# Performance work log

Measured on AMD Instinct MI355X. Metric: run time of the kernel, lower is better.

## Reference

```python
import jax, jax.numpy as jnp
import numpy as np
import math

D = 2048
NH = 16
DH = D // NH
LAT = D // 4
B, S = 2, 2048
EPS = 1e-5


def _ln(x, g, b):
    m = jnp.mean(x, axis=-1, keepdims=True)
    v = jnp.mean((x - m) ** 2, axis=-1, keepdims=True)
    return (x - m) * jax.lax.rsqrt(v + EPS) * g + b


def setup_inputs() -> dict:
    key = jax.random.key(0)
    ks = jax.random.split(key, 12)
    p = lambda k, shape: 0.01 * jax.random.normal(k, shape, dtype=jnp.float32)
    return {
        "x": jax.random.normal(ks[0], (B, S, D), dtype=jnp.float32),
        "W_dq": p(ks[1], (D, LAT)),
        "W_uq": p(ks[2], (LAT, D)),
        "q_ln_g": jnp.ones((LAT,), jnp.float32),
        "q_ln_b": jnp.zeros((LAT,), jnp.float32),
        "W_dkv": p(ks[3], (D, LAT)),
        "W_ukv": p(ks[4], (LAT, 2 * D)),
        "kv_ln_g": jnp.ones((LAT,), jnp.float32),
        "kv_ln_b": jnp.zeros((LAT,), jnp.float32),
        "W_o": p(ks[5], (D, D)),
        "norm1_g": jnp.ones((D,), jnp.float32),
        "norm1_b": jnp.zeros((D,), jnp.float32),
        "norm2_g": jnp.ones((D,), jnp.float32),
        "norm2_b": jnp.zeros((D,), jnp.float32),
        "fc1_w": p(ks[6], (4 * D, D)),
        "fc1_b": jnp.zeros((4 * D,), jnp.float32),
        "fc2_w": p(ks[7], (D, 4 * D)),
        "fc2_b": jnp.zeros((D,), jnp.float32),
    }


def reference(x, W_dq, W_uq, q_ln_g, q_ln_b, W_dkv, W_ukv, kv_ln_g, kv_ln_b,
              W_o, norm1_g, norm1_b, norm2_g, norm2_b, fc1_w, fc1_b, fc2_w, fc2_b):
    normed = _ln(x, norm1_g, norm1_b)

    # --- RopelessMLA attention ---
    cq = _ln(normed @ W_dq, q_ln_g, q_ln_b)          # [B,S,LAT]
    Q = cq @ W_uq                                     # [B,S,D]
    ckv = _ln(normed @ W_dkv, kv_ln_g, kv_ln_b)       # [B,S,LAT]
    KV = ckv @ W_ukv                                  # [B,S,2D]
    K, V = KV[..., :D], KV[..., D:]

    q = Q.reshape(B, S, NH, DH)
    k = K.reshape(B, S, NH, DH)
    v = V.reshape(B, S, NH, DH)

    qkt = jnp.einsum("bqhd,bkhd->bhqk", q, k) / math.sqrt(float(DH))
    mask = jnp.tril(jnp.ones((S, S), dtype=qkt.dtype))  # causal, past_length=0
    qkt = qkt * mask
    qkt = jnp.where(qkt == 0.0, -jnp.inf, qkt)  # faithful to original zero->-inf trick
    attn = jax.nn.softmax(qkt, axis=-1)
    o = jnp.einsum("bhqk,bkhd->bqhd", attn, v).reshape(B, S, D)
    mh_x = o @ W_o.T

    x = x + mh_x
    h = _ln(x, norm2_g, norm2_b)
    h = jax.nn.relu(h @ fc1_w.T + fc1_b)
    h = h @ fc2_w.T + fc2_b  # dropout is identity in eval mode
    return x + h
```

## Files before the change

### kernel.cpp

```cpp
#include <hip/hip_runtime.h>
#include <hip/hip_bf16.h>


#define DEVI __device__ __forceinline__

typedef __attribute__((ext_vector_type(8))) short bf16x8;
typedef __attribute__((ext_vector_type(4))) float f32x4;

DEVI unsigned short f2bf(float f) {
  union { float f; unsigned u; } v; v.f = f;
  unsigned r = v.u + 0x7fffu + ((v.u >> 16) & 1u);
  return (unsigned short)(r >> 16);
}

DEVI float bf2f(unsigned short u) {
  union { unsigned u; float f; } v; v.u = ((unsigned)u) << 16;
  return v.f;
}

#define GLDS16(gp, lp)                                              \
  __builtin_amdgcn_global_load_lds(                                 \
      (__attribute__((address_space(1))) void*)(gp),                \
      (__attribute__((address_space(3))) void*)(lp), 16, 0, 0)

#define NEG_INF (-__builtin_inff())

__global__ __launch_bounds__(256) void cast_f32_bf16(
    const float* __restrict__ in, unsigned short* __restrict__ out, long n) {
  long i = ((long)blockIdx.x * 256 + threadIdx.x) * 4;
  if (i >= n) return;
  const float4 v = *reinterpret_cast<const float4*>(in + i);
  ushort4 o;
  o.x = f2bf(v.x); o.y = f2bf(v.y); o.z = f2bf(v.z); o.w = f2bf(v.w);
  *reinterpret_cast<ushort4*>(out + i) = o;
}

__global__ __launch_bounds__(256) void transpose_cast(
    const float* __restrict__ in, unsigned short* __restrict__ out, int R, int C) {
  __shared__ float tile[32][33];
  const int c0 = blockIdx.x * 32, r0 = blockIdx.y * 32;
  const int tx = threadIdx.x & 31, ty = threadIdx.x >> 5;
#pragma unroll
  for (int i = 0; i < 32; i += 8)
    tile[ty + i][tx] = in[(long)(r0 + ty + i) * C + c0 + tx];
  __syncthreads();
#pragma unroll
  for (int i = 0; i < 32; i += 8)
    out[(long)(c0 + ty + i) * R + r0 + tx] = f2bf(tile[tx][ty + i]);
}

__global__ __launch_bounds__(256) void v_transpose(
    const unsigned short* __restrict__ KV, unsigned short* __restrict__ Vt) {
  __shared__ unsigned short sh[32][33];
  const int s0 = blockIdx.x * 32, d0 = blockIdx.y * 32, bh = blockIdx.z;
  const int b = bh >> 4, h = bh & 15;
  const int tx = threadIdx.x & 31, ty = threadIdx.x >> 5;
#pragma unroll
  for (int i = 0; i < 32; i += 8)
    sh[ty + i][tx] = KV[((long)(b * 2048 + s0 + ty + i)) * 4096 + 2048 + h * 128 + d0 + tx];
  __syncthreads();
#pragma unroll
  for (int i = 0; i < 32; i += 8)
    Vt[((long)(bh * 128 + d0 + ty + i)) * 2048 + s0 + tx] = sh[tx][ty + i];
}

DEVI float blockReduceSum(float v) {
  v += __shfl_xor(v, 1);  v += __shfl_xor(v, 2);  v += __shfl_xor(v, 4);
  v += __shfl_xor(v, 8);  v += __shfl_xor(v, 16); v += __shfl_xor(v, 32);
  __shared__ float red[4];
  if ((threadIdx.x & 63) == 0) red[threadIdx.x >> 6] = v;
  __syncthreads();
  v = red[0] + red[1] + red[2] + red[3];
  __syncthreads();
  return v;
}

template <int W>
__global__ __launch_bounds__(256) void layernorm_bf16(
    const float* __restrict__ in, const float* __restrict__ g,
    const float* __restrict__ b, unsigned short* __restrict__ out, int ldin) {
  constexpr int VPT = W / 256;
  const long row = blockIdx.x;
  const float* x = in + row * ldin;
  float v[VPT];
  float s = 0.f;
#pragma unroll
  for (int i = 0; i < VPT; i++) { v[i] = x[threadIdx.x + i * 256]; s += v[i]; }
  s = blockReduceSum(s);
  const float mean = s * (1.0f / W);
  float s2 = 0.f;
#pragma unroll
  for (int i = 0; i < VPT; i++) { float d = v[i] - mean; s2 += d * d; }
  s2 = blockReduceSum(s2);
  const float rstd = rsqrtf(s2 * (1.0f / W) + 1e-5f);
#pragma unroll
  for (int i = 0; i < VPT; i++) {
    const int c = threadIdx.x + i * 256;
    out[row * W + c] = f2bf((v[i] - mean) * rstd * g[c] + b[c]);
  }
}

template <bool BIAS, bool RELU, bool RES, bool OBF16>
__global__ __launch_bounds__(256) void gemm_bt(
    const unsigned short* __restrict__ A, const unsigned short* __restrict__ Bt,
    const float* __restrict__ bias, const float* __restrict__ res,
    void* __restrict__ Cout, int M, int N, int K) {
  __shared__ __align__(16) unsigned short As[2][128 * 32];
  __shared__ __align__(16) unsigned short Bs[2][128 * 32];

  const int m0 = blockIdx.x * 128;
  const int n0 = blockIdx.y * 128;
  const int tid = threadIdx.x;
  const int lane = tid & 63, w = tid >> 6;
  const int wr = (w >> 1) * 64, wc = (w & 1) * 64;
  const int lrow = lane & 15, lk = (lane >> 4) * 8;

  f32x4 acc[4][4] = {};

  const int nt = K >> 5;
  const int r_ = (tid * 8) >> 5;
  const int c_ = (tid * 8) & 31;

#define STAGE(buf, t)                                                        \
  {                                                                          \
    const long k0 = (long)(t) * 32;                                          \
    GLDS16(A + (long)(m0 + r_) * K + k0 + c_, &As[buf][tid * 8]);            \
    GLDS16(A + (long)(m0 + 64 + r_) * K + k0 + c_, &As[buf][2048 + tid * 8]);\
    GLDS16(Bt + (long)(n0 + r_) * K + k0 + c_, &Bs[buf][tid * 8]);           \
    GLDS16(Bt + (long)(n0 + 64 + r_) * K + k0 + c_, &Bs[buf][2048 + tid * 8]);\
  }

  STAGE(0, 0)
  __syncthreads();
  int cur = 0;
  for (int t = 0; t < nt; t++) {
    if (t + 1 < nt) STAGE(cur ^ 1, t + 1)
    bf16x8 fa[4], fb[4];
#pragma unroll
    for (int i = 0; i < 4; i++) {
      fa[i] = *reinterpret_cast<const bf16x8*>(&As[cur][(wr + i * 16 + lrow) * 32 + lk]);
      fb[i] = *reinterpret_cast<const bf16x8*>(&Bs[cur][(wc + i * 16 + lrow) * 32 + lk]);
    }
#pragma unroll
    for (int i = 0; i < 4; i++)
#pragma unroll
      for (int j = 0; j < 4; j++)
        acc[i][j] = __builtin_amdgcn_mfma_f32_16x16x32_bf16(fa[i], fb[j], acc[i][j], 0, 0, 0);
    __syncthreads();
    cur ^= 1;
  }
#undef STAGE

#pragma unroll
  for (int i = 0; i < 4; i++) {
#pragma unroll
    for (int j = 0; j < 4; j++) {
      const int row = m0 + wr + i * 16 + ((lane >> 4) << 2);
      const int col = n0 + wc + j * 16 + lrow;
      float bv = 0.f;
      if (BIAS) bv = bias[col];
#pragma unroll
      for (int r = 0; r < 4; r++) {
        float v = acc[i][j][r];
        const long idx = (long)(row + r) * N + col;
        if (BIAS) v += bv;
        if (RELU) v = fmaxf(v, 0.f);
        if (RES) v += res[idx];
        if (OBF16) ((unsigned short*)Cout)[idx] = f2bf(v);
        else       ((float*)Cout)[idx] = v;
      }
    }
  }
}

template <bool BIAS, bool RELU, bool OBF16>
__global__ __launch_bounds__(512, 1) void gemm256p(
    const unsigned short* __restrict__ A, const unsigned short* __restrict__ Bt,
    const float* __restrict__ bias, void* __restrict__ Cout,
    int M, int N, int lda, int ldb, int kLen, long kOff) {
  __shared__ __align__(16) unsigned short L[2][2][2][256 * 32];

  const int m0 = blockIdx.x * 256, n0 = blockIdx.y * 256;
  const long ka = (long)blockIdx.z * kOff;
  const int tid = threadIdx.x;
  const int lane = tid & 63, w = tid >> 6;
  const int wm = w >> 2, wn = w & 3;
  const int g = lane >> 4, lrow = lane & 15;

  f32x4 acc[8][4] = {};
  const int nt = kLen >> 6;

#define STG(b, ab, kh, t, P, base0, ld)                                        \
  {                                                                            \
    const long k0 = ka + (long)(t) * 64 + (kh) * 32;                           \
    { const int o = tid;       const int r = o >> 2, s = o & 3;                \
      GLDS16((P) + (long)((base0) + r) * (ld) + k0 + ((s ^ ((r >> 1) & 3)) << 3), \
             &L[b][ab][kh][o * 8]); }                                          \
    { const int o = 512 + tid; const int r = o >> 2, s = o & 3;                \
      GLDS16((P) + (long)((base0) + r) * (ld) + k0 + ((s ^ ((r >> 1) & 3)) << 3), \
             &L[b][ab][kh][o * 8]); }                                          \
  }

#define RD_A(dst, Ahalf, qm)                                                   \
  _Pragma("unroll")                                                            \
  for (int i = 0; i < 4; i++) {                                                \
    const int r = wm * 128 + (qm) * 64 + i * 16 + lrow;                        \
    dst[i] = *reinterpret_cast<const bf16x8*>(                                 \
        &(Ahalf)[(r * 4 + (g ^ ((r >> 1) & 3))) * 8]);                         \
  }
#define RD_B(dst, Bhalf)                                                       \
  _Pragma("unroll")                                                            \
  for (int j = 0; j < 4; j++) {                                                \
    const int r = wn * 64 + j * 16 + lrow;                                     \
    dst[j] = *reinterpret_cast<const bf16x8*>(                                 \
        &(Bhalf)[(r * 4 + (g ^ ((r >> 1) & 3))) * 8]);                         \
  }
#define MFMA16(qm)                                                             \
  __builtin_amdgcn_s_setprio(1);                                               \
  _Pragma("unroll")                                                            \
  for (int i = 0; i < 4; i++)                                                  \
    _Pragma("unroll")                                                          \
    for (int j = 0; j < 4; j++)                                                \
      acc[(qm) * 4 + i][j] = __builtin_amdgcn_mfma_f32_16x16x32_bf16(          \
          fa[i], fb[j], acc[(qm) * 4 + i][j], 0, 0, 0);                        \
  __builtin_amdgcn_s_setprio(0);

  STG(0, 0, 0, 0, A, m0, lda)
  STG(0, 1, 0, 0, Bt, n0, ldb)
  STG(0, 0, 1, 0, A, m0, lda)
  STG(0, 1, 1, 0, Bt, n0, ldb)
  asm volatile("s_waitcnt vmcnt(4)\n\ts_barrier" ::: "memory");

  bf16x8 fb[4];
  for (int t = 0; t < nt; t++) {
    const int bu = t & 1, bn = bu ^ 1;
    const bool pf = (t + 1 < nt);
    const unsigned short* A0 = L[bu][0][0];
    const unsigned short* A1 = L[bu][0][1];
    const unsigned short* B0 = L[bu][1][0];
    const unsigned short* B1 = L[bu][1][1];

    {
      bf16x8 fa[4];
      RD_A(fa, A0, 0)
      RD_B(fb, B0)
      if (pf) STG(bn, 0, 0, t + 1, A, m0, lda)
      asm volatile("s_barrier" ::: "memory");
      MFMA16(0)
      asm volatile("s_barrier" ::: "memory");
    }
    {
      bf16x8 fa[4];
      RD_A(fa, A0, 1)
      if (pf) STG(bn, 1, 0, t + 1, Bt, n0, ldb)
      asm volatile("s_barrier" ::: "memory");
      MFMA16(1)
      if (pf) asm volatile("s_waitcnt vmcnt(4)" ::: "memory");
      else    asm volatile("s_waitcnt vmcnt(0)" ::: "memory");
      asm volatile("s_barrier" ::: "memory");
    }
    {
      bf16x8 fa[4];
      RD_A(fa, A1, 0)
      RD_B(fb, B1)
      if (pf) STG(bn, 0, 1, t + 1, A, m0, lda)
      asm volatile("s_barrier" ::: "memory");
      MFMA16(0)
      asm volatile("s_barrier" ::: "memory");
    }
    {
      bf16x8 fa[4];
      RD_A(fa, A1, 1)
      if (pf) STG(bn, 1, 1, t + 1, Bt, n0, ldb)
      asm volatile("s_barrier" ::: "memory");
      MFMA16(1)
      if (pf) asm volatile("s_waitcnt vmcnt(4)" ::: "memory");
      else    asm volatile("s_waitcnt vmcnt(0)" ::: "memory");
      asm volatile("s_barrier" ::: "memory");
    }
  }
#undef STG
#undef RD_A
#undef RD_B
#undef MFMA16

  const long zoff = (long)blockIdx.z * (long)M * (long)N;
#pragma unroll
  for (int i = 0; i < 8; i++) {
#pragma unroll
    for (int j = 0; j < 4; j++) {
      const int row = m0 + wm * 128 + i * 16 + g * 4;
      const int col = n0 + wn * 64 + j * 16 + lrow;
      float bv = 0.f;
      if (BIAS) bv = bias[col];
#pragma unroll
      for (int r = 0; r < 4; r++) {
        float v = acc[i][j][r];
        if (BIAS) v += bv;
        if (RELU) v = fmaxf(v, 0.f);
        const long idx = zoff + (long)(row + r) * N + col;
        if (OBF16) ((unsigned short*)Cout)[idx] = f2bf(v);
        else       ((float*)Cout)[idx] = v;
      }
    }
  }
}

template <bool BIAS>
__global__ __launch_bounds__(256) void combine2(
    const unsigned short* __restrict__ p, const float* __restrict__ bias,
    const float* __restrict__ res, float* __restrict__ out, long n) {
  const long i = ((long)blockIdx.x * 256 + threadIdx.x) * 4;
  if (i >= n) return;
  const ushort4 a = *reinterpret_cast<const ushort4*>(p + i);
  const ushort4 b = *reinterpret_cast<const ushort4*>(p + n + i);
  const float4 r = *reinterpret_cast<const float4*>(res + i);
  float4 o;
  o.x = bf2f(a.x) + bf2f(b.x) + r.x;
  o.y = bf2f(a.y) + bf2f(b.y) + r.y;
  o.z = bf2f(a.z) + bf2f(b.z) + r.z;
  o.w = bf2f(a.w) + bf2f(b.w) + r.w;
  if (BIAS) {
    const int col = (int)(i & 2047);
    const float4 bv = *reinterpret_cast<const float4*>(bias + col);
    o.x += bv.x; o.y += bv.y; o.z += bv.z; o.w += bv.w;
  }
  *reinterpret_cast<float4*>(out + i) = o;
}

__global__ __launch_bounds__(256) void flash_attn(
    const unsigned short* __restrict__ Q, const unsigned short* __restrict__ KV,
    const unsigned short* __restrict__ Vt, unsigned short* __restrict__ O) {
  constexpr int S = 2048;
  const int tid = threadIdx.x, lane = tid & 63, w = tid >> 6;
  const int g = lane >> 4, lcol = lane & 15;
  const int wg = blockIdx.x;
  const int x8 = wg & 7, q64 = wg >> 3;
  const int p = q64 & 15, hi = q64 >> 4;
  const int bh = x8 * 4 + hi;
  const int b = bh >> 4, h = bh & 15;
  const long kvrow0 = (long)b * S;
  const int hd0 = h * 128;

  __shared__ __align__(16) unsigned short Kl[64 * 128];
  __shared__ __align__(16) unsigned short Vl[128 * 64];
  __shared__ __align__(16) unsigned short Pl[4 * 16 * 72];

  const float kscale = 0.08838834764831845f * 1.4426950408889634f;

  for (int ti = 0; ti < 2; ti++) {
    const int t = ti ? (31 - p) : p;
    const int qbase = t * 64;
    bf16x8 qf[4];
#pragma unroll
    for (int dc = 0; dc < 4; dc++)
      qf[dc] = *reinterpret_cast<const bf16x8*>(
          Q + (kvrow0 + qbase + w * 16 + lcol) * 2048 + hd0 + dc * 32 + g * 8);
    f32x4 oacc[8] = {};
    float mst[4] = {NEG_INF, NEG_INF, NEG_INF, NEG_INF};
    float lst[4] = {0.f, 0.f, 0.f, 0.f};
    const int nk = t + 1;
    for (int kt = 0; kt < nk; kt++) {
      const int kv0 = kt * 64;
      __syncthreads();
#pragma unroll
      for (int i = 0; i < 4; i++) {
        const int o16 = i * 256 + tid;
        const int kr = o16 >> 4, ks = o16 & 15;
        GLDS16(KV + (kvrow0 + kv0 + kr) * 4096 + hd0 + 8 * (ks ^ (kr & 7)),
               Kl + o16 * 8);
        const int vd = o16 >> 3, vs = o16 & 7;
        GLDS16(Vt + ((long)bh * 128 + vd) * 2048 + kv0 + 8 * (vs ^ (vd & 7)),
               Vl + o16 * 8);
      }
      __syncthreads();
      f32x4 sc[4] = {};
      __builtin_amdgcn_s_setprio(1);
#pragma unroll
      for (int dc = 0; dc < 4; dc++) {
#pragma unroll
        for (int c = 0; c < 4; c++) {
          const bf16x8 kf = *reinterpret_cast<const bf16x8*>(
              Kl + (c * 16 + lcol) * 128 + 8 * ((4 * dc + g) ^ (lcol & 7)));
          sc[c] = __builtin_amdgcn_mfma_f32_16x16x32_bf16(qf[dc], kf, sc[c], 0, 0, 0);
        }
      }
      __builtin_amdgcn_s_setprio(0);
      float s[4][4];
      const int qrow = qbase + w * 16 + g * 4;
      if (kt == nk - 1) {
#pragma unroll
        for (int c = 0; c < 4; c++) {
          const int col = kv0 + c * 16 + lcol;
#pragma unroll
          for (int r = 0; r < 4; r++)
            s[c][r] = (col <= qrow + r) ? sc[c][r] * kscale : NEG_INF;
        }
      } else {
#pragma unroll
        for (int c = 0; c < 4; c++)
#pragma unroll
          for (int r = 0; r < 4; r++) s[c][r] = sc[c][r] * kscale;
      }
      float pm[4];
#pragma unroll
      for (int r = 0; r < 4; r++) {
        float mx = fmaxf(fmaxf(s[0][r], s[1][r]), fmaxf(s[2][r], s[3][r]));
        mx = fmaxf(mx, __shfl_xor(mx, 1));
        mx = fmaxf(mx, __shfl_xor(mx, 2));
        mx = fmaxf(mx, __shfl_xor(mx, 4));
        mx = fmaxf(mx, __shfl_xor(mx, 8));
        pm[r] = mx;
      }
      bool need = false;
#pragma unroll
      for (int r = 0; r < 4; r++) need = need || (pm[r] > mst[r] + 11.5f);
      if (__any(need)) {
#pragma unroll
        for (int r = 0; r < 4; r++) {
          const float mnew = fmaxf(mst[r], pm[r]);
          const float corr = exp2f(mst[r] - mnew);
          mst[r] = mnew;
          lst[r] *= corr;
#pragma unroll
          for (int db = 0; db < 8; db++) oacc[db][r] *= corr;
        }
      }
#pragma unroll
      for (int r = 0; r < 4; r++) {
        float ps = 0.f;
#pragma unroll
        for (int c = 0; c < 4; c++) {
          const float pv = exp2f(s[c][r] - mst[r]);
          Pl[(w * 16 + g * 4 + r) * 72 + c * 16 + lcol] = f2bf(pv);
          ps += pv;
        }
        ps += __shfl_xor(ps, 1); ps += __shfl_xor(ps, 2);
        ps += __shfl_xor(ps, 4); ps += __shfl_xor(ps, 8);
        lst[r] += ps;
      }
      __builtin_amdgcn_s_setprio(1);
#pragma unroll
      for (int kk = 0; kk < 2; kk++) {
        const bf16x8 pf = *reinterpret_cast<const bf16x8*>(
            Pl + (w * 16 + lcol) * 72 + kk * 32 + g * 8);
#pragma unroll
        for (int db = 0; db < 8; db++) {
          const bf16x8 vf = *reinterpret_cast<const bf16x8*>(
              Vl + (db * 16 + lcol) * 64 + 8 * ((4 * kk + g) ^ (lcol & 7)));
          oacc[db] = __builtin_amdgcn_mfma_f32_16x16x32_bf16(pf, vf, oacc[db], 0, 0, 0);
        }
      }
      __builtin_amdgcn_s_setprio(0);
    }
#pragma unroll
    for (int db = 0; db < 8; db++)
#pragma unroll
      for (int r = 0; r < 4; r++) {
        const int qi = qbase + w * 16 + g * 4 + r;
        O[(kvrow0 + qi) * 2048 + hd0 + db * 16 + lcol] = f2bf(oacc[db][r] / lst[r]);
      }
  }
}

extern "C" void kernel_launch(void* const* d_in, const int* in_sizes, int n_in,
                              void* d_out, int out_size, void* d_ws, size_t ws_size,
                              hipStream_t stream) {
  (void)in_sizes; (void)n_in; (void)out_size; (void)ws_size;
  const float* x     = (const float*)d_in[0];
  const float* W_dq  = (const float*)d_in[1];
  const float* W_uq  = (const float*)d_in[2];
  const float* qlng  = (const float*)d_in[3];
  const float* qlnb  = (const float*)d_in[4];
  const float* W_dkv = (const float*)d_in[5];
  const float* W_ukv = (const float*)d_in[6];
  const float* klng  = (const float*)d_in[7];
  const float* klnb  = (const float*)d_in[8];
  const float* W_o   = (const float*)d_in[9];
  const float* n1g   = (const float*)d_in[10];
  const float* n1b   = (const float*)d_in[11];
  const float* n2g   = (const float*)d_in[12];
  const float* n2b   = (const float*)d_in[13];
  const float* fc1w  = (const float*)d_in[14];
  const float* fc1b  = (const float*)d_in[15];
  const float* fc2w  = (const float*)d_in[16];
  const float* fc2b  = (const float*)d_in[17];
  float* out = (float*)d_out;

  char* ws = (char*)d_ws;
  unsigned short* normed = (unsigned short*)(ws + 0);
  unsigned short* Obuf   = (unsigned short*)(ws + 0);
  unsigned short* fc2bb  = (unsigned short*)(ws + 0);
  float*          cqkv_pre = (float*)(ws + 33554432);
  unsigned short* KV       = (unsigned short*)(ws + 33554432);
  unsigned short* fc1bb    = (unsigned short*)(ws + 33554432);
  unsigned short* fc2part  = (unsigned short*)(ws + 33554432);
  unsigned short* cq  = (unsigned short*)(ws + 67108864);
  unsigned short* Qb = (unsigned short*)(ws + 71303168);
  unsigned short* h1 = (unsigned short*)(ws + 71303168);
  unsigned short* ckv = (unsigned short*)(ws + 88080384);
  float* x2           = (float*)(ws + 88080384);
  unsigned short* Vtb    = (unsigned short*)(ws + 121634816);
  unsigned short* wopart = (unsigned short*)(ws + 121634816);
  unsigned short* hmid   = (unsigned short*)(ws + 121634816);
  unsigned short* dqkv_t = (unsigned short*)(ws + 188743680);
  unsigned short* uq_t   = dqkv_t + 2097152;
  unsigned short* ukv_t  = uq_t + 1048576;
  unsigned short* wo_b   = ukv_t + 2097152;

  const dim3 blk(256);
  const dim3 blk8(512);

  transpose_cast<<<dim3(512 / 32, 2048 / 32), blk, 0, stream>>>(W_dq, dqkv_t, 2048, 512);
  transpose_cast<<<dim3(512 / 32, 2048 / 32), blk, 0, stream>>>(W_dkv, dqkv_t + 512 * 2048, 2048, 512);
  transpose_cast<<<dim3(2048 / 32, 512 / 32), blk, 0, stream>>>(W_uq, uq_t, 512, 2048);
  transpose_cast<<<dim3(4096 / 32, 512 / 32), blk, 0, stream>>>(W_ukv, ukv_t, 512, 4096);
  cast_f32_bf16<<<2048 * 2048 / 1024, blk, 0, stream>>>(W_o, wo_b, 2048 * 2048);

  layernorm_bf16<2048><<<4096, blk, 0, stream>>>(x, n1g, n1b, normed, 2048);
  gemm_bt<false, false, false, false><<<dim3(32, 8), blk, 0, stream>>>(
      normed, dqkv_t, nullptr, nullptr, cqkv_pre, 4096, 1024, 2048);
  layernorm_bf16<512><<<4096, blk, 0, stream>>>(cqkv_pre, qlng, qlnb, cq, 1024);
  layernorm_bf16<512><<<4096, blk, 0, stream>>>(cqkv_pre + 512, klng, klnb, ckv, 1024);
  gemm_bt<false, false, false, true><<<dim3(32, 16), blk, 0, stream>>>(
      cq, uq_t, nullptr, nullptr, Qb, 4096, 2048, 512);
  gemm256p<false, false, true><<<dim3(16, 16), blk8, 0, stream>>>(
      ckv, ukv_t, nullptr, KV, 4096, 4096, 512, 512, 512, 0);
  v_transpose<<<dim3(64, 4, 32), blk, 0, stream>>>(KV, Vtb);
  flash_attn<<<dim3(512), blk, 0, stream>>>(Qb, KV, Vtb, Obuf);
  cast_f32_bf16<<<8192 * 2048 / 1024, blk, 0, stream>>>(fc1w, fc1bb, 8192L * 2048);
  gemm256p<false, false, true><<<dim3(16, 8, 2), blk8, 0, stream>>>(
      Obuf, wo_b, nullptr, wopart, 4096, 2048, 2048, 2048, 1024, 1024);
  cast_f32_bf16<<<2048 * 8192 / 1024, blk, 0, stream>>>(fc2w, fc2bb, 2048L * 8192);
  combine2<false><<<8192, blk, 0, stream>>>(wopart, nullptr, x, x2, 8388608L);
  layernorm_bf16<2048><<<4096, blk, 0, stream>>>(x2, n2g, n2b, h1, 2048);
  gemm256p<true, true, true><<<dim3(16, 32), blk8, 0, stream>>>(
      h1, fc1bb, fc1b, hmid, 4096, 8192, 2048, 2048, 2048, 0);
  gemm256p<false, false, true><<<dim3(16, 8, 2), blk8, 0, stream>>>(
      hmid, fc2bb, nullptr, fc2part, 4096, 2048, 8192, 8192, 4096, 4096);
  combine2<true><<<8192, blk, 0, stream>>>(fc2part, fc2b, x2, out, 8388608L);
}
```

Baseline: 598.7 us.

## Restructure gemm256p K-loop barriers and fuse split-K combine with layernorm

Rewrites the gemm256p inner loop from four barrier-separated quarter phases into two k-halves. Each half loads all A and B fragments, issues both the A and B prefetches, then runs 32 MFMAs under a single barrier. This cuts the number of s_barrier syncs per K tile and gives longer uninterrupted MFMA runs, at the cost of more live fragment registers. It also fuses the split-K partial combine with the residual add and the second layernorm into one kernel, saving a launch and a round trip of x2 through global memory.

```diff
diff --git a/kernel.cpp b/kernel.cpp
--- a/kernel.cpp
+++ b/kernel.cpp
@@ -100,6 +100,50 @@
   }
 }
 
+__global__ __launch_bounds__(256) void combine_ln(
+    const unsigned short* __restrict__ p, const float* __restrict__ xres,
+    const float* __restrict__ g, const float* __restrict__ b,
+    float* __restrict__ x2, unsigned short* __restrict__ h1, long n) {
+  const int c0 = threadIdx.x * 8;
+  const long base = (long)blockIdx.x * 2048 + c0;
+  float v[8];
+  float s = 0.f;
+#pragma unroll
+  for (int hh = 0; hh < 2; hh++) {
+    const long i = base + hh * 4;
+    const ushort4 a  = *reinterpret_cast<const ushort4*>(p + i);
+    const ushort4 bb = *reinterpret_cast<const ushort4*>(p + n + i);
+    const float4 r = *reinterpret_cast<const float4*>(xres + i);
+    float4 o;
+    o.x = r.x + bf2f(a.x) + bf2f(bb.x);
+    o.y = r.y + bf2f(a.y) + bf2f(bb.y);
+    o.z = r.z + bf2f(a.z) + bf2f(bb.z);
+    o.w = r.w + bf2f(a.w) + bf2f(bb.w);
+    *reinterpret_cast<float4*>(x2 + i) = o;
+    v[hh * 4 + 0] = o.x; v[hh * 4 + 1] = o.y;
+    v[hh * 4 + 2] = o.z; v[hh * 4 + 3] = o.w;
+    s += o.x + o.y + o.z + o.w;
+  }
+  s = blockReduceSum(s);
+  const float mean = s * (1.0f / 2048.f);
+  float s2 = 0.f;
+#pragma unroll
+  for (int i = 0; i < 8; i++) { float d = v[i] - mean; s2 += d * d; }
+  s2 = blockReduceSum(s2);
+  const float rstd = rsqrtf(s2 * (1.0f / 2048.f) + 1e-5f);
+#pragma unroll
+  for (int hh = 0; hh < 2; hh++) {
+    const float4 gv = *reinterpret_cast<const float4*>(g + c0 + hh * 4);
+    const float4 bv = *reinterpret_cast<const float4*>(b + c0 + hh * 4);
+    ushort4 o;
+    o.x = f2bf((v[hh * 4 + 0] - mean) * rstd * gv.x + bv.x);
+    o.y = f2bf((v[hh * 4 + 1] - mean) * rstd * gv.y + bv.y);
+    o.z = f2bf((v[hh * 4 + 2] - mean) * rstd * gv.z + bv.z);
+    o.w = f2bf((v[hh * 4 + 3] - mean) * rstd * gv.w + bv.w);
+    *reinterpret_cast<ushort4*>(h1 + base + hh * 4) = o;
+  }
+}
+
 template <bool BIAS, bool RELU, bool RES, bool OBF16>
 __global__ __launch_bounds__(256) void gemm_bt(
     const unsigned short* __restrict__ A, const unsigned short* __restrict__ Bt,
@@ -215,15 +259,6 @@
     dst[j] = *reinterpret_cast<const bf16x8*>(                                 \
         &(Bhalf)[(r * 4 + (g ^ ((r >> 1) & 3))) * 8]);                         \
   }
-#define MFMA16(qm)                                                             \
-  __builtin_amdgcn_s_setprio(1);                                               \
-  _Pragma("unroll")                                                            \
-  for (int i = 0; i < 4; i++)                                                  \
-    _Pragma("unroll")                                                          \
-    for (int j = 0; j < 4; j++)                                                \
-      acc[(qm) * 4 + i][j] = __builtin_amdgcn_mfma_f32_16x16x32_bf16(          \
-          fa[i], fb[j], acc[(qm) * 4 + i][j], 0, 0, 0);                        \
-  __builtin_amdgcn_s_setprio(0);
 
   STG(0, 0, 0, 0, A, m0, lda)
   STG(0, 1, 0, 0, Bt, n0, ldb)
@@ -231,58 +266,44 @@
   STG(0, 1, 1, 0, Bt, n0, ldb)
   asm volatile("s_waitcnt vmcnt(4)\n\ts_barrier" ::: "memory");
 
-  bf16x8 fb[4];
   for (int t = 0; t < nt; t++) {
     const int bu = t & 1, bn = bu ^ 1;
     const bool pf = (t + 1 < nt);
-    const unsigned short* A0 = L[bu][0][0];
-    const unsigned short* A1 = L[bu][0][1];
-    const unsigned short* B0 = L[bu][1][0];
-    const unsigned short* B1 = L[bu][1][1];
-
-    {
-      bf16x8 fa[4];
-      RD_A(fa, A0, 0)
-      RD_B(fb, B0)
-      if (pf) STG(bn, 0, 0, t + 1, A, m0, lda)
-      asm volatile("s_barrier" ::: "memory");
-      MFMA16(0)
-      asm volatile("s_barrier" ::: "memory");
-    }
-    {
-      bf16x8 fa[4];
-      RD_A(fa, A0, 1)
-      if (pf) STG(bn, 1, 0, t + 1, Bt, n0, ldb)
-      asm volatile("s_barrier" ::: "memory");
-      MFMA16(1)
-      if (pf) asm volatile("s_waitcnt vmcnt(4)" ::: "memory");
-      else    asm volatile("s_waitcnt vmcnt(0)" ::: "memory");
-      asm volatile("s_barrier" ::: "memory");
-    }
-    {
-      bf16x8 fa[4];
-      RD_A(fa, A1, 0)
-      RD_B(fb, B1)
-      if (pf) STG(bn, 0, 1, t + 1, A, m0, lda)
-      asm volatile("s_barrier" ::: "memory");
-      MFMA16(0)
-      asm volatile("s_barrier" ::: "memory");
-    }
-    {
-      bf16x8 fa[4];
-      RD_A(fa, A1, 1)
-      if (pf) STG(bn, 1, 1, t + 1, Bt, n0, ldb)
-      asm volatile("s_barrier" ::: "memory");
-      MFMA16(1)
-      if (pf) asm volatile("s_waitcnt vmcnt(4)" ::: "memory");
-      else    asm volatile("s_waitcnt vmcnt(0)" ::: "memory");
-      asm volatile("s_barrier" ::: "memory");
+#pragma unroll
+    for (int kh = 0; kh < 2; kh++) {
+      const unsigned short* Ah = L[bu][0][kh];
+      const unsigned short* Bh = L[bu][1][kh];
+      bf16x8 fa[4], fa2[4], fb[4];
+      RD_A(fa, Ah, 0)
+      RD_B(fb, Bh)
+      RD_A(fa2, Ah, 1)
+      if (pf) {
+        STG(bn, 0, kh, t + 1, A, m0, lda)
+        STG(bn, 1, kh, t + 1, Bt, n0, ldb)
+      }
+      __builtin_amdgcn_s_setprio(1);
+#pragma unroll
+      for (int i = 0; i < 4; i++)
+#pragma unroll
+        for (int j = 0; j < 4; j++)
+          acc[i][j] = __builtin_amdgcn_mfma_f32_16x16x32_bf16(fa[i], fb[j], acc[i][j], 0, 0, 0);
+#pragma unroll
+      for (int i = 0; i < 4; i++)
+#pragma unroll
+        for (int j = 0; j < 4; j++)
+          acc[4 + i][j] = __builtin_amdgcn_mfma_f32_16x16x32_bf16(fa2[i], fb[j], acc[4 + i][j], 0, 0, 0);
+      __builtin_amdgcn_s_setprio(0);
+      if (kh == 0) {
+        if (pf) asm volatile("s_waitcnt vmcnt(4)\n\ts_barrier" ::: "memory");
+        else    asm volatile("s_waitcnt vmcnt(0)\n\ts_barrier" ::: "memory");
+      } else if (pf) {
+        asm volatile("s_waitcnt vmcnt(4) lgkmcnt(0)\n\ts_barrier" ::: "memory");
+      }
     }
   }
 #undef STG
 #undef RD_A
 #undef RD_B
-#undef MFMA16
 
   const long zoff = (long)blockIdx.z * (long)M * (long)N;
 #pragma unroll
@@ -532,8 +553,7 @@
   gemm256p<false, false, true><<<dim3(16, 8, 2), blk8, 0, stream>>>(
       Obuf, wo_b, nullptr, wopart, 4096, 2048, 2048, 2048, 1024, 1024);
   cast_f32_bf16<<<2048 * 8192 / 1024, blk, 0, stream>>>(fc2w, fc2bb, 2048L * 8192);
-  combine2<false><<<8192, blk, 0, stream>>>(wopart, nullptr, x, x2, 8388608L);
-  layernorm_bf16<2048><<<4096, blk, 0, stream>>>(x2, n2g, n2b, h1, 2048);
+  combine_ln<<<4096, blk, 0, stream>>>(wopart, x, n2g, n2b, x2, h1, 8388608L);
   gemm256p<true, true, true><<<dim3(16, 32), blk8, 0, stream>>>(
       h1, fc1bb, fc1b, hmid, 4096, 8192, 2048, 2048, 2048, 0);
   gemm256p<false, false, true><<<dim3(16, 8, 2), blk8, 0, stream>>>(
```

New measurement: 581.3 us. 2.9% less time.
